# Performance work log

Hardware: AMD Instinct MI355X
Metric: run time of the kernel (lower is better)

Reference implementation:

```python
import jax, jax.numpy as jnp
import numpy as np

H = 16      # how_many_heads
DH = 64     # dimension_of_head
D_K = 1024  # dimension_of_key (input dim); scaler = sqrt(D_K), faithful to source
NEG = -np.finfo(np.float32).max


def setup_inputs() -> dict:
    key0 = jax.random.key(0)
    ks = jax.random.split(key0, 8)
    B, S, D = 2, 2048, 1024
    query = jax.random.normal(ks[0], (B, S, D), dtype=jnp.float32)
    key_in = jax.random.normal(ks[1], (B, S, D), dtype=jnp.float32)
    value = jax.random.normal(ks[2], (B, S, D), dtype=jnp.float32)
    mask = jax.random.bernoulli(ks[3], 0.5, (B, S, S))  # bool, True = masked
    # nn.Linear(in, out, bias=False): y = x @ W^T with W:[out,in]; store [in,out] directly
    sc = 1.0 / np.sqrt(D)
    W_q = jax.random.normal(ks[4], (D, H * DH), dtype=jnp.float32) * sc
    W_k = jax.random.normal(ks[5], (D, H * DH), dtype=jnp.float32) * sc
    W_v = jax.random.normal(ks[6], (D, H * DH), dtype=jnp.float32) * sc
    W_o = jax.random.normal(ks[7], (H * DH, D), dtype=jnp.float32) * sc
    return {"query": query, "key": key_in, "value": value, "mask": mask,
            "W_q": W_q, "W_k": W_k, "W_v": W_v, "W_o": W_o}


def reference(query, key, value, mask, W_q, W_k, W_v, W_o):
    B, Sq, _ = query.shape
    # project and split heads: [B, S, H, DH] -> [B, H, S, DH]
    q = (query @ W_q).reshape(B, Sq, H, DH).transpose(0, 2, 1, 3)
    k = (key @ W_k).reshape(B, -1, H, DH).transpose(0, 2, 1, 3)
    v = (value @ W_v).reshape(B, -1, H, DH).transpose(0, 2, 1, 3)
    # scores: [B, H, Sq, Sk], scaled by sqrt(dimension_of_key)=sqrt(D_K)
    scores = jnp.einsum('bhqd,bhkd->bhqk', q, k) / np.float32(np.sqrt(D_K))
    # mask: [B, Sq, Sk] -> [B, H, Sq, Sk]; masked_fill with -finfo(float32).max
    scores = jnp.where(mask[:, None, :, :], NEG, scores)
    # FAITHFUL to source: softmax over dim=2 (the QUERY axis of the 4D tensor)
    attn = jax.nn.softmax(scores, axis=2)
    hidden = jnp.einsum('bhqk,bhkd->bhqd', attn, v)  # [B, H, Sq, DH]
    hidden = hidden.transpose(0, 2, 1, 3).reshape(B, Sq, H * DH) @ W_o
    return hidden, k, v
```

## Files before the change

### kernel.cpp

```cpp
#include <hip/hip_runtime.h>
#include <hip/hip_bf16.h>

#define BB 2
#define SS 2048
#define DD 1024
#define HH 16
#define DHH 64

#define SCLOG2E 0.045084221f

typedef unsigned short u16;
typedef unsigned int   u32;
typedef __bf16 bf16_t;
typedef bf16_t bf16x8 __attribute__((ext_vector_type(8)));
typedef u16    u16x8  __attribute__((ext_vector_type(8)));
typedef u32    u32x4v __attribute__((ext_vector_type(4)));
typedef float  f32x4  __attribute__((ext_vector_type(4)));

#define MFMA(a,b,c) __builtin_amdgcn_mfma_f32_16x16x32_bf16(a,b,c,0,0,0)

#define SW(c,r)  ((c) ^ ((r) & 7))
#define SW3(c,r) ((c) ^ ((r) & 3))

typedef __attribute__((address_space(1))) const unsigned int as1_u32;
typedef __attribute__((address_space(3))) unsigned int as3_u32;

__device__ __forceinline__ void gld16(const void* g, void* l){
  __builtin_amdgcn_global_load_lds((as1_u32*)g, (as3_u32*)l, 16, 0, 0);
}

__device__ __forceinline__ u16 f2bf(float f){
  u32 u = __builtin_bit_cast(u32, f);
  u32 r = (u + 0x7fffu + ((u >> 16) & 1u)) >> 16;
  return (u16)r;
}
__device__ __forceinline__ u16 nbf(float f){
  bf16_t b = (bf16_t)f;
  return __builtin_bit_cast(u16, b);
}
__device__ __forceinline__ float bf2f(u16 v){
  u32 u = ((u32)v) << 16;
  return __builtin_bit_cast(float, u);
}
__device__ __forceinline__ bf16x8 ldb8(const u16* p){
  return __builtin_bit_cast(bf16x8, *(const u16x8*)p);
}

__device__ __forceinline__ void stage64(const u16* __restrict__ g0, int stride,
                                        u16* lds0, int tid){
  int w = tid >> 6, lane = tid & 63;
  #pragma unroll
  for (int j = 0; j < 2; j++){
    int slot = j*256 + w*64 + lane;
    int row = slot >> 3, c = slot & 7;
    gld16(g0 + (size_t)row*stride + (SW(c,row) << 3),
          lds0 + (size_t)(j*256 + w*64)*8);
  }
}

__device__ __forceinline__ void stage32(const u16* __restrict__ g0, int stride,
                                        u16* lds0, int tid){
  int w = tid >> 6, lane = tid & 63;
  #pragma unroll
  for (int j = 0; j < 2; j++){
    int slot = j*256 + w*64 + lane;
    int row = slot >> 2, c = slot & 3;
    gld16(g0 + (size_t)row*stride + (SW3(c,row) << 3),
          lds0 + (size_t)(j*256 + w*64)*8);
  }
}

__global__ __launch_bounds__(256) void cvt3(const float* __restrict__ s0,
                                            const float* __restrict__ s1,
                                            const float* __restrict__ s2,
                                            u16* __restrict__ d0,
                                            u16* __restrict__ d1,
                                            u16* __restrict__ d2){
  const float* s = blockIdx.z == 0 ? s0 : (blockIdx.z == 1 ? s1 : s2);
  u16*         d = blockIdx.z == 0 ? d0 : (blockIdx.z == 1 ? d1 : d2);
  size_t i = ((size_t)blockIdx.x*256 + threadIdx.x) * 8;
  const float4* p = (const float4*)(s + i);
  float4 x = p[0], y = p[1];
  u16x8 u;
  u[0]=f2bf(x.x); u[1]=f2bf(x.y); u[2]=f2bf(x.z); u[3]=f2bf(x.w);
  u[4]=f2bf(y.x); u[5]=f2bf(y.y); u[6]=f2bf(y.z); u[7]=f2bf(y.w);
  *(u16x8*)(d + i) = u;
}

__global__ __launch_bounds__(256) void detect_mask(const u32* mw, u32* flag){
  __shared__ int fBig, fFloat;
  if (threadIdx.x == 0){ fBig = 0; fFloat = 0; }
  __syncthreads();
  for (int i = threadIdx.x; i < 4096; i += 256){
    u32 w = mw[i];
    if (w == 0x3f800000u) fFloat = 1;
    else if (w > 1u) fBig = 1;
  }
  __syncthreads();
  if (threadIdx.x == 0) *flag = fFloat ? 2u : (fBig ? 1u : 0u);
}

__global__ __launch_bounds__(256) void pack_mask(const void* __restrict__ mask,
                                                 const u32* __restrict__ flag,
                                                 u32* __restrict__ pm){
  int w = blockIdx.x * 256 + threadIdx.x;
  if (w >= BB*SS*(SS/32)) return;
  u32 f = *flag;
  size_t e0 = (size_t)w * 32;
  u32 bits = 0;
  if (f == 1u){
    const uchar4* mb = (const uchar4*)((const unsigned char*)mask + e0);
    #pragma unroll
    for (int j = 0; j < 8; j++){
      uchar4 v = mb[j];
      bits |= (v.x?1u:0u) << (4*j)   | (v.y?1u:0u) << (4*j+1)
            | (v.z?1u:0u) << (4*j+2) | (v.w?1u:0u) << (4*j+3);
    }
  } else if (f == 0u){
    const int4* mi = (const int4*)((const int*)mask + e0);
    #pragma unroll
    for (int j = 0; j < 8; j++){
      int4 v = mi[j];
      bits |= (v.x?1u:0u) << (4*j)   | (v.y?1u:0u) << (4*j+1)
            | (v.z?1u:0u) << (4*j+2) | (v.w?1u:0u) << (4*j+3);
    }
  } else {
    const float4* mf = (const float4*)((const float*)mask + e0);
    #pragma unroll
    for (int j = 0; j < 8; j++){
      float4 v = mf[j];
      bits |= (v.x!=0.f?1u:0u) << (4*j)   | (v.y!=0.f?1u:0u) << (4*j+1)
            | (v.z!=0.f?1u:0u) << (4*j+2) | (v.w!=0.f?1u:0u) << (4*j+3);
    }
  }
  pm[w] = bits;
}

__global__ __launch_bounds__(256) void prep_w(const float* __restrict__ W0,
                                              const float* __restrict__ W1,
                                              const float* __restrict__ W2,
                                              const float* __restrict__ W3,
                                              u16* __restrict__ Wt){
  const float* Ws[4] = {W0, W1, W2, W3};
  const float* W = Ws[blockIdx.z];
  float scl = (blockIdx.z == 0) ? SCLOG2E : 1.0f;
  u16* O = Wt + (size_t)blockIdx.z * DD * DD;
  __shared__ float tile[64][65];
  int kb = blockIdx.x * 64, nb = blockIdx.y * 64;
  int col = threadIdx.x & 63, rr = threadIdx.x >> 6;
  #pragma unroll
  for (int i = 0; i < 16; i++){
    int row = i*4 + rr;
    tile[row][col] = W[(size_t)(kb+row)*DD + nb + col];
  }
  __syncthreads();
  #pragma unroll
  for (int i = 0; i < 16; i++){
    int row = i*4 + rr;
    O[(size_t)(nb+row)*DD + kb + col] = f2bf(tile[col][row] * scl);
  }
}

struct GA { const u16* A; const u16* Bt; u16* Cb; float* Co; int mode; };

__global__ __launch_bounds__(256) void gemm32(GA a0, GA a1, GA a2){
  GA ga = blockIdx.z == 0 ? a0 : (blockIdx.z == 1 ? a1 : a2);
  __shared__ u16 As[2][128*32];
  __shared__ u16 Bs[2][128*32];
  int mb = blockIdx.x * 128, nb = blockIdx.y * 128;
  int tid = threadIdx.x, w = tid >> 6, lane = tid & 63, ln = lane & 15, g = lane >> 4;
  int wr = w >> 1, wc = w & 1;
  f32x4 acc[4][4];
  #pragma unroll
  for (int i = 0; i < 4; i++)
    #pragma unroll
    for (int j = 0; j < 4; j++) acc[i][j] = (f32x4){0,0,0,0};

  stage32(ga.A  + (size_t)mb*DD, DD, As[0], tid);
  stage32(ga.Bt + (size_t)nb*DD, DD, Bs[0], tid);
  __syncthreads();
  int buf = 0;
  for (int t = 0; t < 32; t++){
    if (t < 31){
      stage32(ga.A  + (size_t)mb*DD + (t+1)*32, DD, As[buf^1], tid);
      stage32(ga.Bt + (size_t)nb*DD + (t+1)*32, DD, Bs[buf^1], tid);
    }
    bf16x8 av[4], bv[4];
    #pragma unroll
    for (int mf = 0; mf < 4; mf++){
      int row = wr*64 + mf*16 + ln;
      av[mf] = ldb8(&As[buf][row*32 + (SW3(g,row) << 3)]);
    }
    #pragma unroll
    for (int nf = 0; nf < 4; nf++){
      int row = wc*64 + nf*16 + ln;
      bv[nf] = ldb8(&Bs[buf][row*32 + (SW3(g,row) << 3)]);
    }
    #pragma unroll
    for (int mf = 0; mf < 4; mf++)
      #pragma unroll
      for (int nf = 0; nf < 4; nf++)
        acc[mf][nf] = MFMA(av[mf], bv[nf], acc[mf][nf]);
    __syncthreads();
    buf ^= 1;
  }
  #pragma unroll
  for (int mf = 0; mf < 4; mf++){
    #pragma unroll
    for (int nf = 0; nf < 4; nf++){
      #pragma unroll
      for (int r = 0; r < 4; r++){
        int row = mb + wr*64 + mf*16 + g*4 + r;
        int col = nb + wc*64 + nf*16 + ln;
        float v = acc[mf][nf][r];
        if (ga.mode != 2)
          ga.Cb[(size_t)row*DD + col] = f2bf(v);
        if (ga.mode == 1){
          int b_ = row >> 11, s_ = row & (SS-1);
          int h_ = col >> 6,  d_ = col & 63;
          ga.Co[(((size_t)(b_*HH + h_))*SS + s_)*DHH + d_] = v;
        }
        if (ga.mode == 2)
          ga.Co[(size_t)row*DD + col] = v;
      }
    }
  }
}

__global__ __launch_bounds__(256) void pass1_sum(const u16* __restrict__ Qb,
                                                 const u16* __restrict__ Kb,
                                                 const u32* __restrict__ pm,
                                                 float* __restrict__ cO){
  __shared__ u16 Qst[2][64*64];
  int flat = blockIdx.x + (SS/128)*(blockIdx.y + HH*blockIdx.z);
  int sw = (flat & 7)*64 + (flat >> 3);
  int kblk = (sw & 15) * 128;
  int rest = sw >> 4;
  int h = rest & 15, b = rest >> 4;
  int tid = threadIdx.x, w = tid >> 6, lane = tid & 63, ln = lane & 15, g = lane >> 4;
  bf16x8 kf[2][2];
  #pragma unroll
  for (int f = 0; f < 2; f++){
    const u16* kp = Kb + ((size_t)b*SS + kblk + w*32 + f*16 + ln)*DD + h*DHH + g*8;
    kf[f][0] = ldb8(kp); kf[f][1] = ldb8(kp + 32);
  }
  float cr[2][4] = {{0,0,0,0},{0,0,0,0}};

  stage64(Qb + ((size_t)b*SS)*DD + h*DHH, DD, Qst[0], tid);
  __syncthreads();
  int buf = 0;
  size_t kwbase = (size_t)(b*SS)*(SS/32) + (kblk >> 5) + w;
  for (int t = 0; t < 32; t++){
    if (t < 31) stage64(Qb + ((size_t)b*SS + (t+1)*64)*DD + h*DHH, DD, Qst[buf^1], tid);
    #pragma unroll
    for (int qc = 0; qc < 4; qc++){
      int row = qc*16 + ln;
      bf16x8 b0 = ldb8(&Qst[buf][row*64 + (SW(g,  row) << 3)]);
      bf16x8 b1 = ldb8(&Qst[buf][row*64 + (SW(g+4,row) << 3)]);
      int q = t*64 + qc*16 + ln;
      u32 mw = pm[(size_t)q*(SS/32) + kwbase];
      #pragma unroll
      for (int f = 0; f < 2; f++){
        f32x4 sf = {0,0,0,0};
        sf = MFMA(kf[f][0], b0, sf);
        sf = MFMA(kf[f][1], b1, sf);
        #pragma unroll
        for (int r = 0; r < 4; r++){
          float e = __builtin_amdgcn_exp2f(sf[r]);
          cr[f][r] += ((mw >> (f*16 + g*4 + r)) & 1u) ? 0.f : e;
        }
      }
    }
    __syncthreads();
    buf ^= 1;
  }
  #pragma unroll
  for (int f = 0; f < 2; f++)
    #pragma unroll
    for (int r = 0; r < 4; r++){
      #pragma unroll
      for (int msk = 1; msk < 16; msk <<= 1)
        cr[f][r] += __shfl_xor(cr[f][r], msk, 64);
    }
  if (ln == 0){
    #pragma unroll
    for (int f = 0; f < 2; f++)
      #pragma unroll
      for (int r = 0; r < 4; r++)
        cO[((size_t)b*HH + h)*SS + kblk + w*32 + f*16 + g*4 + r] = cr[f][r];
  }
}

__global__ __launch_bounds__(256) void scale_v(const u16* __restrict__ Vb,
                                               const float* __restrict__ cI,
                                               u16* __restrict__ Vt){
  int b = blockIdx.z, h = blockIdx.y;
  int st = blockIdx.x * 64;
  __shared__ u16 tile[64][72];
  int col = threadIdx.x & 63, rr = threadIdx.x >> 6;
  #pragma unroll
  for (int i = 0; i < 16; i++){
    int row = i*4 + rr;
    int s = st + row;
    float inv = 1.0f / cI[((size_t)b*HH + h)*SS + s];
    float v = bf2f(Vb[((size_t)b*SS + s)*DD + h*DHH + col]);
    tile[row][col] = f2bf(v * inv);
  }
  __syncthreads();
  int pc = (col & 32) + ((col >> 2) & 3)*8 + ((col >> 4) & 1)*4 + (col & 3);
  #pragma unroll
  for (int i = 0; i < 16; i++){
    int row = i*4 + rr;
    Vt[(((size_t)b*HH + h)*DHH + row)*SS + st + pc] = tile[col][row];
  }
}

__global__ __launch_bounds__(256) void pass2_pv(const u16* __restrict__ Qb,
                                                const u16* __restrict__ Kb,
                                                const u16* __restrict__ Vt,
                                                const u32* __restrict__ pm,
                                                u16* __restrict__ Hb){
  __shared__ u16 Kst[2][64*64];
  __shared__ u16 Vst[2][64*64];
  int flat = blockIdx.x + (SS/128)*(blockIdx.y + HH*blockIdx.z);
  int sw = (flat & 7)*64 + (flat >> 3);
  int qt = (sw & 15) * 128;
  int rest = sw >> 4;
  int h = rest & 15, b = rest >> 4;
  int tid = threadIdx.x, w = tid >> 6, lane = tid & 63, ln = lane & 15, g = lane >> 4;
  bf16x8 qf[2][2];
  #pragma unroll
  for (int f = 0; f < 2; f++){
    const u16* qp = Qb + ((size_t)b*SS + qt + w*32 + f*16 + ln)*DD + h*DHH + g*8;
    qf[f][0] = ldb8(qp); qf[f][1] = ldb8(qp + 32);
  }
  f32x4 acc[2][4];
  #pragma unroll
  for (int f = 0; f < 2; f++)
    #pragma unroll
    for (int d = 0; d < 4; d++) acc[f][d] = (f32x4){0,0,0,0};

  const u16* Kg  = Kb + ((size_t)b*SS)*DD + h*DHH;
  const u16* Vth = Vt + ((size_t)b*HH + h)*DHH*SS;
  const u32* pmr[2];
  #pragma unroll
  for (int f = 0; f < 2; f++)
    pmr[f] = pm + ((size_t)b*SS + qt + w*32 + f*16 + ln)*(SS/32);

  stage64(Kg,  DD, Kst[0], tid);
  stage64(Vth, SS, Vst[0], tid);
  __syncthreads();
  int buf = 0;
  for (int t = 0; t < 32; t++){
    if (t < 31){
      stage64(Kg + (size_t)(t+1)*64*DD, DD, Kst[buf^1], tid);
      stage64(Vth + (t+1)*64,           SS, Vst[buf^1], tid);
    }
    u32 mlo[2], mhi[2];
    #pragma unroll
    for (int f = 0; f < 2; f++){ mlo[f] = pmr[f][t*2]; mhi[f] = pmr[f][t*2+1]; }
    u32 pk[2][8];
    #pragma unroll
    for (int kc = 0; kc < 4; kc++){
      int row = kc*16 + ln;
      bf16x8 a0 = ldb8(&Kst[buf][row*64 + (SW(g,  row) << 3)]);
      bf16x8 a1 = ldb8(&Kst[buf][row*64 + (SW(g+4,row) << 3)]);
      #pragma unroll
      for (int f = 0; f < 2; f++){
        f32x4 sf = {0,0,0,0};
        sf = MFMA(a0, qf[f][0], sf);
        sf = MFMA(a1, qf[f][1], sf);
        u32 mword = (kc < 2) ? mlo[f] : mhi[f];
        int msh = (kc & 1) * 16 + g*4;
        float p0 = ((mword >> (msh+0)) & 1u) ? 0.f : __builtin_amdgcn_exp2f(sf[0]);
        float p1 = ((mword >> (msh+1)) & 1u) ? 0.f : __builtin_amdgcn_exp2f(sf[1]);
        float p2 = ((mword >> (msh+2)) & 1u) ? 0.f : __builtin_amdgcn_exp2f(sf[2]);
        float p3 = ((mword >> (msh+3)) & 1u) ? 0.f : __builtin_amdgcn_exp2f(sf[3]);
        pk[f][kc*2]   = (u32)nbf(p0) | ((u32)nbf(p1) << 16);
        pk[f][kc*2+1] = (u32)nbf(p2) | ((u32)nbf(p3) << 16);
      }
    }
    #pragma unroll
    for (int kh = 0; kh < 2; kh++){
      bf16x8 pa[2];
      #pragma unroll
      for (int f = 0; f < 2; f++)
        pa[f] = __builtin_bit_cast(bf16x8,
          (u32x4v){pk[f][4*kh], pk[f][4*kh+1], pk[f][4*kh+2], pk[f][4*kh+3]});
      #pragma unroll
      for (int df = 0; df < 4; df++){
        int row = df*16 + ln;
        bf16x8 bv = ldb8(&Vst[buf][row*64 + (SW(kh*4+g, row) << 3)]);
        #pragma unroll
        for (int f = 0; f < 2; f++)
          acc[f][df] = MFMA(pa[f], bv, acc[f][df]);
      }
    }
    __syncthreads();
    buf ^= 1;
  }
  #pragma unroll
  for (int f = 0; f < 2; f++)
    #pragma unroll
    for (int df = 0; df < 4; df++)
      #pragma unroll
      for (int r = 0; r < 4; r++){
        int row = qt + w*32 + f*16 + g*4 + r;
        int col = h*DHH + df*16 + ln;
        Hb[((size_t)b*SS + row)*DD + col] = f2bf(acc[f][df][r]);
      }
}

extern "C" void kernel_launch(void* const* d_in, const int* in_sizes, int n_in,
                              void* d_out, int out_size, void* d_ws, size_t ws_size,
                              hipStream_t stream){
  (void)in_sizes; (void)n_in; (void)out_size; (void)ws_size;
  const float* query = (const float*)d_in[0];
  const float* key   = (const float*)d_in[1];
  const float* value = (const float*)d_in[2];
  const void*  mask  = d_in[3];
  const float* W_q = (const float*)d_in[4];
  const float* W_k = (const float*)d_in[5];
  const float* W_v = (const float*)d_in[6];
  const float* W_o = (const float*)d_in[7];

  float* out   = (float*)d_out;
  float* out_h = out;
  float* out_k = out   + (size_t)BB*HH*SS*DHH;
  float* out_v = out_k + (size_t)BB*HH*SS*DHH;

  char* w = (char*)d_ws;
  u16*   Wt  = (u16*)(w);
  u16*   Av  = (u16*)(w + (size_t)( 8u<<20));
  u16*   Qb  = (u16*)(w + (size_t)(16u<<20));
  u16*   Kb  = (u16*)(w + (size_t)(24u<<20));
  u16*   Vb  = (u16*)(w + (size_t)(32u<<20));
  u16*   Vt  = (u16*)(w + (size_t)(40u<<20));
  float* cS  = (float*)(w + (size_t)(48u<<20));
  u32*   pm  = (u32*)(w + (size_t)(48u<<20) + (512u<<10));
  u32*   flag= (u32*)(w + (size_t)(48u<<20) + (1664u<<10));
  u16*   Hb  = Av;
  u16*   Aq  = (u16*)out_h;
  u16*   Ak  = Aq + (size_t)BB*SS*DD;

  detect_mask<<<dim3(1), dim3(256), 0, stream>>>((const u32*)mask, flag);
  pack_mask<<<dim3(1024), dim3(256), 0, stream>>>(mask, flag, pm);
  prep_w<<<dim3(16,16,4), dim3(256), 0, stream>>>(W_q, W_k, W_v, W_o, Wt);

  cvt3<<<dim3(2048,1,3), dim3(256), 0, stream>>>(query, key, value, Aq, Ak, Av);

  GA gq = { Aq, Wt,             Qb, nullptr, 0 };
  GA gk = { Ak, Wt + 1*1048576, Kb, out_k,   1 };
  GA gv = { Av, Wt + 2*1048576, Vb, out_v,   1 };
  gemm32<<<dim3(32,8,3), dim3(256), 0, stream>>>(gq, gk, gv);

  pass1_sum<<<dim3(SS/128, HH, BB), dim3(256), 0, stream>>>(Qb, Kb, pm, cS);
  scale_v<<<dim3(SS/64, HH, BB), dim3(256), 0, stream>>>(Vb, cS, Vt);
  pass2_pv<<<dim3(SS/128, HH, BB), dim3(256), 0, stream>>>(Qb, Kb, Vt, pm, Hb);

  GA go = { Hb, Wt + 3*1048576, nullptr, out_h, 2 };
  gemm32<<<dim3(32,8,1), dim3(256), 0, stream>>>(go, go, go);
}
```

Measured before the change: 216.4 us.

## Transpose packed mask layout and software-pipeline QK/PV in pass2 with triple buffering

The packed bitmask is stored transposed (key-word major, query minor), so mask loads in pass1 and pass2 become coalesced across lanes instead of strided by SS/32 words. pass2_pv switches to a three-deep LDS ring for K and V. It computes the QK^T and exp for tile t+1 while issuing the PV MFMAs for tile t, keeping two register sets of packed probabilities. This aims to overlap exp/VALU work with MFMA and hide global staging latency, at the cost of more LDS, more registers and possible occupancy loss.

```diff
diff --git a/kernel.cpp b/kernel.cpp
--- a/kernel.cpp
+++ b/kernel.cpp
@@ -100,13 +100,16 @@
   if (threadIdx.x == 0) *flag = fFloat ? 2u : (fBig ? 1u : 0u);
 }
 
-__global__ __launch_bounds__(256) void pack_mask(const void* __restrict__ mask,
-                                                 const u32* __restrict__ flag,
-                                                 u32* __restrict__ pm){
+__global__ __launch_bounds__(256) void pack_maskT(const void* __restrict__ mask,
+                                                  const u32* __restrict__ flag,
+                                                  u32* __restrict__ pmT){
   int w = blockIdx.x * 256 + threadIdx.x;
-  if (w >= BB*SS*(SS/32)) return;
+  if (w >= BB*64*SS) return;
   u32 f = *flag;
-  size_t e0 = (size_t)w * 32;
+  int q  = w & (SS-1);
+  int kw = (w >> 11) & 63;
+  int b  = w >> 17;
+  size_t e0 = ((size_t)(b*SS + q))*SS + kw*32;
   u32 bits = 0;
   if (f == 1u){
     const uchar4* mb = (const uchar4*)((const unsigned char*)mask + e0);
@@ -133,7 +136,7 @@
             | (v.z!=0.f?1u:0u) << (4*j+2) | (v.w!=0.f?1u:0u) << (4*j+3);
     }
   }
-  pm[w] = bits;
+  pmT[w] = bits;
 }
 
 __global__ __launch_bounds__(256) void prep_w(const float* __restrict__ W0,
@@ -229,7 +232,7 @@
 
 __global__ __launch_bounds__(256) void pass1_sum(const u16* __restrict__ Qb,
                                                  const u16* __restrict__ Kb,
-                                                 const u32* __restrict__ pm,
+                                                 const u32* __restrict__ pmT,
                                                  float* __restrict__ cO){
   __shared__ u16 Qst[2][64*64];
   int flat = blockIdx.x + (SS/128)*(blockIdx.y + HH*blockIdx.z);
@@ -249,7 +252,7 @@
   stage64(Qb + ((size_t)b*SS)*DD + h*DHH, DD, Qst[0], tid);
   __syncthreads();
   int buf = 0;
-  size_t kwbase = (size_t)(b*SS)*(SS/32) + (kblk >> 5) + w;
+  const u32* pmw = pmT + ((size_t)b*64 + (kblk >> 5) + w)*SS;
   for (int t = 0; t < 32; t++){
     if (t < 31) stage64(Qb + ((size_t)b*SS + (t+1)*64)*DD + h*DHH, DD, Qst[buf^1], tid);
     #pragma unroll
@@ -258,7 +261,7 @@
       bf16x8 b0 = ldb8(&Qst[buf][row*64 + (SW(g,  row) << 3)]);
       bf16x8 b1 = ldb8(&Qst[buf][row*64 + (SW(g+4,row) << 3)]);
       int q = t*64 + qc*16 + ln;
-      u32 mw = pm[(size_t)q*(SS/32) + kwbase];
+      u32 mw = pmw[q];
       #pragma unroll
       for (int f = 0; f < 2; f++){
         f32x4 sf = {0,0,0,0};
@@ -315,13 +318,60 @@
   }
 }
 
+#define P2_QK(TT, NXT, KP) { \
+  u32 _ml[2], _mh[2]; \
+  _Pragma("unroll") for (int f = 0; f < 2; f++){ \
+    _ml[f] = pmb[(size_t)(2*(TT))*SS + f*16]; \
+    _mh[f] = pmb[(size_t)(2*(TT)+1)*SS + f*16]; \
+  } \
+  _Pragma("unroll") for (int kc = 0; kc < 4; kc++){ \
+    bf16x8 a0 = ldb8(&KP[koff[kc][0]]); \
+    bf16x8 a1 = ldb8(&KP[koff[kc][1]]); \
+    _Pragma("unroll") for (int f = 0; f < 2; f++){ \
+      f32x4 sf = {0,0,0,0}; \
+      sf = MFMA(a0, qf[f][0], sf); \
+      sf = MFMA(a1, qf[f][1], sf); \
+      u32 mword = (kc < 2) ? _ml[f] : _mh[f]; \
+      int msh = (kc & 1) * 16 + g*4; \
+      float p0 = ((mword >> (msh+0)) & 1u) ? 0.f : __builtin_amdgcn_exp2f(sf[0]); \
+      float p1 = ((mword >> (msh+1)) & 1u) ? 0.f : __builtin_amdgcn_exp2f(sf[1]); \
+      float p2 = ((mword >> (msh+2)) & 1u) ? 0.f : __builtin_amdgcn_exp2f(sf[2]); \
+      float p3 = ((mword >> (msh+3)) & 1u) ? 0.f : __builtin_amdgcn_exp2f(sf[3]); \
+      NXT[f][kc*2]   = (u32)nbf(p0) | ((u32)nbf(p1) << 16); \
+      NXT[f][kc*2+1] = (u32)nbf(p2) | ((u32)nbf(p3) << 16); \
+    } \
+  } }
+
+#define P2_PV(CUR, VP) \
+  _Pragma("unroll") for (int kh = 0; kh < 2; kh++){ \
+    bf16x8 pa[2]; \
+    _Pragma("unroll") for (int f = 0; f < 2; f++) \
+      pa[f] = __builtin_bit_cast(bf16x8, \
+        (u32x4v){CUR[f][4*kh], CUR[f][4*kh+1], CUR[f][4*kh+2], CUR[f][4*kh+3]}); \
+    _Pragma("unroll") for (int df = 0; df < 4; df++){ \
+      bf16x8 bv = ldb8(&VP[voff[kh][df]]); \
+      _Pragma("unroll") for (int f = 0; f < 2; f++) \
+        acc[f][df] = MFMA(pa[f], bv, acc[f][df]); \
+    } \
+  }
+
+#define P2_BODY(TT, CUR, NXT) \
+  __syncthreads(); \
+  if ((TT) < 30){ \
+    stage64(Kg + (size_t)((TT)+2)*64*DD, DD, K2, tid); \
+    stage64(Vth + ((TT)+2)*64,           SS, V2, tid); \
+  } \
+  if ((TT) < 31) P2_QK((TT)+1, NXT, K1) \
+  P2_PV(CUR, V0) \
+  { u16* _tp=K0; K0=K1; K1=K2; K2=_tp; _tp=V0; V0=V1; V1=V2; V2=_tp; }
+
 __global__ __launch_bounds__(256) void pass2_pv(const u16* __restrict__ Qb,
                                                 const u16* __restrict__ Kb,
                                                 const u16* __restrict__ Vt,
-                                                const u32* __restrict__ pm,
+                                                const u32* __restrict__ pmT,
                                                 u16* __restrict__ Hb){
-  __shared__ u16 Kst[2][64*64];
-  __shared__ u16 Vst[2][64*64];
+  __shared__ u16 Kst[3][64*64];
+  __shared__ u16 Vst[3][64*64];
   int flat = blockIdx.x + (SS/128)*(blockIdx.y + HH*blockIdx.z);
   int sw = (flat & 7)*64 + (flat >> 3);
   int qt = (sw & 15) * 128;
@@ -342,63 +392,40 @@
 
   const u16* Kg  = Kb + ((size_t)b*SS)*DD + h*DHH;
   const u16* Vth = Vt + ((size_t)b*HH + h)*DHH*SS;
-  const u32* pmr[2];
-  #pragma unroll
-  for (int f = 0; f < 2; f++)
-    pmr[f] = pm + ((size_t)b*SS + qt + w*32 + f*16 + ln)*(SS/32);
-
-  stage64(Kg,  DD, Kst[0], tid);
-  stage64(Vth, SS, Vst[0], tid);
-  __syncthreads();
-  int buf = 0;
-  for (int t = 0; t < 32; t++){
-    if (t < 31){
-      stage64(Kg + (size_t)(t+1)*64*DD, DD, Kst[buf^1], tid);
-      stage64(Vth + (t+1)*64,           SS, Vst[buf^1], tid);
-    }
-    u32 mlo[2], mhi[2];
-    #pragma unroll
-    for (int f = 0; f < 2; f++){ mlo[f] = pmr[f][t*2]; mhi[f] = pmr[f][t*2+1]; }
-    u32 pk[2][8];
-    #pragma unroll
-    for (int kc = 0; kc < 4; kc++){
-      int row = kc*16 + ln;
-      bf16x8 a0 = ldb8(&Kst[buf][row*64 + (SW(g,  row) << 3)]);
-      bf16x8 a1 = ldb8(&Kst[buf][row*64 + (SW(g+4,row) << 3)]);
-      #pragma unroll
-      for (int f = 0; f < 2; f++){
-        f32x4 sf = {0,0,0,0};
-        sf = MFMA(a0, qf[f][0], sf);
-        sf = MFMA(a1, qf[f][1], sf);
-        u32 mword = (kc < 2) ? mlo[f] : mhi[f];
-        int msh = (kc & 1) * 16 + g*4;
-        float p0 = ((mword >> (msh+0)) & 1u) ? 0.f : __builtin_amdgcn_exp2f(sf[0]);
-        float p1 = ((mword >> (msh+1)) & 1u) ? 0.f : __builtin_amdgcn_exp2f(sf[1]);
-        float p2 = ((mword >> (msh+2)) & 1u) ? 0.f : __builtin_amdgcn_exp2f(sf[2]);
-        float p3 = ((mword >> (msh+3)) & 1u) ? 0.f : __builtin_amdgcn_exp2f(sf[3]);
-        pk[f][kc*2]   = (u32)nbf(p0) | ((u32)nbf(p1) << 16);
-        pk[f][kc*2+1] = (u32)nbf(p2) | ((u32)nbf(p3) << 16);
-      }
-    }
-    #pragma unroll
-    for (int kh = 0; kh < 2; kh++){
-      bf16x8 pa[2];
-      #pragma unroll
-      for (int f = 0; f < 2; f++)
-        pa[f] = __builtin_bit_cast(bf16x8,
-          (u32x4v){pk[f][4*kh], pk[f][4*kh+1], pk[f][4*kh+2], pk[f][4*kh+3]});
-      #pragma unroll
-      for (int df = 0; df < 4; df++){
-        int row = df*16 + ln;
-        bf16x8 bv = ldb8(&Vst[buf][row*64 + (SW(kh*4+g, row) << 3)]);
-        #pragma unroll
-        for (int f = 0; f < 2; f++)
-          acc[f][df] = MFMA(pa[f], bv, acc[f][df]);
-      }
-    }
-    __syncthreads();
-    buf ^= 1;
-  }
+  const u32* pmb = pmT + (size_t)b*64*SS + (qt + w*32 + ln);
+
+  int koff[4][2], voff[2][4];
+  #pragma unroll
+  for (int kc = 0; kc < 4; kc++){
+    int row = kc*16 + ln;
+    koff[kc][0] = row*64 + (SW(g,  row) << 3);
+    koff[kc][1] = row*64 + (SW(g+4,row) << 3);
+  }
+  #pragma unroll
+  for (int kh = 0; kh < 2; kh++)
+    #pragma unroll
+    for (int df = 0; df < 4; df++){
+      int row = df*16 + ln;
+      voff[kh][df] = row*64 + (SW(kh*4+g, row) << 3);
+    }
+
+  u16 *K0=&Kst[0][0], *K1=&Kst[1][0], *K2=&Kst[2][0];
+  u16 *V0=&Vst[0][0], *V1=&Vst[1][0], *V2=&Vst[2][0];
+  u32 pkA[2][8], pkB[2][8];
+
+  stage64(Kg,  DD, K0, tid);
+  stage64(Vth, SS, V0, tid);
+  __syncthreads();
+  P2_QK(0, pkA, K0)
+  stage64(Kg + 64*DD, DD, K1, tid);
+  stage64(Vth + 64,   SS, V1, tid);
+
+  #pragma unroll 1
+  for (int t = 0; t < 32; t += 2){
+    P2_BODY(t,   pkA, pkB)
+    P2_BODY(t+1, pkB, pkA)
+  }
+
   #pragma unroll
   for (int f = 0; f < 2; f++)
     #pragma unroll
@@ -437,14 +464,14 @@
   u16*   Vb  = (u16*)(w + (size_t)(32u<<20));
   u16*   Vt  = (u16*)(w + (size_t)(40u<<20));
   float* cS  = (float*)(w + (size_t)(48u<<20));
-  u32*   pm  = (u32*)(w + (size_t)(48u<<20) + (512u<<10));
+  u32*   pmT = (u32*)(w + (size_t)(48u<<20) + (512u<<10));
   u32*   flag= (u32*)(w + (size_t)(48u<<20) + (1664u<<10));
   u16*   Hb  = Av;
   u16*   Aq  = (u16*)out_h;
   u16*   Ak  = Aq + (size_t)BB*SS*DD;
 
   detect_mask<<<dim3(1), dim3(256), 0, stream>>>((const u32*)mask, flag);
-  pack_mask<<<dim3(1024), dim3(256), 0, stream>>>(mask, flag, pm);
+  pack_maskT<<<dim3(1024), dim3(256), 0, stream>>>(mask, flag, pmT);
   prep_w<<<dim3(16,16,4), dim3(256), 0, stream>>>(W_q, W_k, W_v, W_o, Wt);
 
   cvt3<<<dim3(2048,1,3), dim3(256), 0, stream>>>(query, key, value, Aq, Ak, Av);
@@ -454,9 +481,9 @@
   GA gv = { Av, Wt + 2*1048576, Vb, out_v,   1 };
   gemm32<<<dim3(32,8,3), dim3(256), 0, stream>>>(gq, gk, gv);
 
-  pass1_sum<<<dim3(SS/128, HH, BB), dim3(256), 0, stream>>>(Qb, Kb, pm, cS);
+  pass1_sum<<<dim3(SS/128, HH, BB), dim3(256), 0, stream>>>(Qb, Kb, pmT, cS);
   scale_v<<<dim3(SS/64, HH, BB), dim3(256), 0, stream>>>(Vb, cS, Vt);
-  pass2_pv<<<dim3(SS/128, HH, BB), dim3(256), 0, stream>>>(Qb, Kb, Vt, pm, Hb);
+  pass2_pv<<<dim3(SS/128, HH, BB), dim3(256), 0, stream>>>(Qb, Kb, Vt, pmT, Hb);
 
   GA go = { Hb, Wt + 3*1048576, nullptr, out_h, 2 };
   gemm32<<<dim3(32,8,1), dim3(256), 0, stream>>>(go, go, go);
```

Result: no change. 220.1 us (+1.7%).
